# Optimization experiments

Hardware: AMD Instinct MI355X
Metric: run time of the kernel (lower is better)

## Reference

```python
import jax, jax.numpy as jnp
import numpy as np

Q_HEADS, KV_HEADS, HEAD_DIM, WINDOW = 16, 4, 128, 512
HIDDEN = 2048
ROPE_BASE = 10000.0


def _rope_tables(T, head_dim, dtype):
    half = head_dim // 2
    inv_freq = 1.0 / (ROPE_BASE ** (jnp.arange(half, dtype=jnp.float32) / half))
    t = jnp.arange(T, dtype=jnp.float32)
    freqs = jnp.outer(t, inv_freq)  # [T, half]
    return jnp.cos(freqs).astype(dtype), jnp.sin(freqs).astype(dtype)


def _apply_rope(x, cos, sin):
    # x: [B, T, H, D]; cos/sin: [T, D//2] -> broadcast [1, T, 1, D//2]
    c = cos[None, :, None, :]
    s = sin[None, :, None, :]
    x1, x2 = jnp.split(x, 2, axis=-1)
    return jnp.concatenate([x1 * c - x2 * s, x1 * s + x2 * c], axis=-1)


def setup_inputs() -> dict:
    key = jax.random.key(0)
    ks = jax.random.split(key, 5)
    B, T = 1, 4096
    x = jax.random.normal(ks[0], (B, T, HIDDEN), dtype=jnp.float32)
    sc = 0.02
    wq = jax.random.normal(ks[1], (Q_HEADS * HEAD_DIM, HIDDEN), dtype=jnp.float32) * sc
    wk = jax.random.normal(ks[2], (KV_HEADS * HEAD_DIM, HIDDEN), dtype=jnp.float32) * sc
    wv = jax.random.normal(ks[3], (KV_HEADS * HEAD_DIM, HIDDEN), dtype=jnp.float32) * sc
    wo = jax.random.normal(ks[4], (HIDDEN, Q_HEADS * HEAD_DIM), dtype=jnp.float32) * sc
    return {"x": x, "wq": wq, "wk": wk, "wv": wv, "wo": wo}


def reference(x, wq, wk, wv, wo):
    B, T, _ = x.shape
    reps = Q_HEADS // KV_HEADS
    scale = 1.0 / np.sqrt(HEAD_DIM)

    q = jnp.einsum('bth,oh->bto', x, wq).reshape(B, T, Q_HEADS, HEAD_DIM)
    k = jnp.einsum('bth,oh->bto', x, wk).reshape(B, T, KV_HEADS, HEAD_DIM)
    v = jnp.einsum('bth,oh->bto', x, wv).reshape(B, T, KV_HEADS, HEAD_DIM)

    cos, sin = _rope_tables(T, HEAD_DIM, x.dtype)
    q = _apply_rope(q, cos, sin)
    k = _apply_rope(k, cos, sin)

    # GQA without materializing repeated K/V: group q as [B,T,KVH,reps,D]
    qg = q.reshape(B, T, KV_HEADS, reps, HEAD_DIM)
    scores = jnp.einsum('btgrd,bsgd->bgrts', qg, k) * scale  # [B,KVH,reps,T,T]

    idx = jnp.arange(T)
    # allowed: causal (s <= t) AND within window (t - s <= WINDOW)
    allowed = (idx[None, :] <= idx[:, None]) & (idx[:, None] - idx[None, :] <= WINDOW)
    scores = jnp.where(allowed[None, None, None], scores, jnp.finfo(scores.dtype).min)
    probs = jax.nn.softmax(scores, axis=-1)

    out = jnp.einsum('bgrts,bsgd->btgrd', probs, v)  # [B,T,KVH,reps,D]
    out = out.reshape(B, T, Q_HEADS * HEAD_DIM)
    return jnp.einsum('bto,ho->bth', out, wo)
```

## Files before the change

### kernel.cpp

```cpp
#include <hip/hip_runtime.h>

typedef __attribute__((ext_vector_type(8))) short short8;
typedef __attribute__((ext_vector_type(4))) short short4_t;
typedef __attribute__((ext_vector_type(4))) float f32x4;
typedef __attribute__((ext_vector_type(4))) unsigned short u16x4;

__device__ __forceinline__ unsigned short f2b(float f) {
  unsigned int u = __float_as_uint(f);
  u += 0x7fffu + ((u >> 16) & 1u);
  return (unsigned short)(u >> 16);
}
__device__ __forceinline__ float b2f(unsigned short s) {
  return __uint_as_float(((unsigned int)s) << 16);
}
__device__ __forceinline__ void glds16(const void* g, void* l) {
  __builtin_amdgcn_global_load_lds(
      (const __attribute__((address_space(1))) unsigned int*)g,
      (__attribute__((address_space(3))) unsigned int*)l, 16, 0, 0);
}

__global__ __launch_bounds__(256) void cast_all(const float* __restrict__ x,
                                                const float* __restrict__ wq,
                                                const float* __restrict__ wk,
                                                const float* __restrict__ wv,
                                                const float* __restrict__ wo,
                                                unsigned short* __restrict__ dst) {
  const int i = blockIdx.x * 256 + threadIdx.x;
  const float* s;
  int off;
  if (i < 2097152)      { s = x;  off = i; }
  else if (i < 3145728) { s = wq; off = i - 2097152; }
  else if (i < 3407872) { s = wk; off = i - 3145728; }
  else if (i < 3670016) { s = wv; off = i - 3407872; }
  else                  { s = wo; off = i - 3670016; }
  f32x4 v = ((const f32x4*)s)[off];
  u16x4 o;
  o[0] = f2b(v[0]); o[1] = f2b(v[1]); o[2] = f2b(v[2]); o[3] = f2b(v[3]);
  ((u16x4*)dst)[i] = o;
}

__global__ __launch_bounds__(256) void gemm_qkv(const unsigned short* __restrict__ A,
                                                const unsigned short* __restrict__ B,
                                                unsigned short* __restrict__ qb,
                                                unsigned short* __restrict__ kb,
                                                unsigned short* __restrict__ vtg) {
  const int K = 2048;
  __shared__ unsigned short As[128 * 32];
  __shared__ unsigned short Bs[128 * 32];
  const int tid = threadIdx.x;
  const int w = tid >> 6, lane = tid & 63;
  const int quad = lane >> 4, l15 = lane & 15;
  const int m0 = blockIdx.x * 128;
  const int nt = blockIdx.y;
  const int n0 = nt * 128;
  const int mbase = (w >> 1) * 64;
  const f32x4 fzero = {0.f, 0.f, 0.f, 0.f};

  f32x4 acc[4][4];
#pragma unroll
  for (int i = 0; i < 4; i++)
#pragma unroll
    for (int j = 0; j < 4; j++) acc[i][j] = fzero;

  const int srow = w * 16 + (lane >> 2);
  const int scol = (lane & 3) * 8;
  const unsigned short* Ag0 = A + (size_t)(m0 + srow) * K + scol;
  const unsigned short* Ag1 = Ag0 + (size_t)64 * K;
  const unsigned short* Bg0 = B + (size_t)(n0 + srow) * K + scol;
  const unsigned short* Bg1 = Bg0 + (size_t)64 * K;

  for (int k0 = 0; k0 < K; k0 += 32) {
    __syncthreads();
    glds16(Ag0 + k0, &As[w * 512]);
    glds16(Ag1 + k0, &As[2048 + w * 512]);
    glds16(Bg0 + k0, &Bs[w * 512]);
    glds16(Bg1 + k0, &Bs[2048 + w * 512]);
    __syncthreads();
    short8 af[4], bf[4];
#pragma unroll
    for (int mi = 0; mi < 4; mi++)
      af[mi] = *(const short8*)&As[(mbase + mi * 16 + l15) * 32 + quad * 8];
#pragma unroll
    for (int ni = 0; ni < 4; ni++) {
      const int ngrp = (w & 1) * 2 + (ni & 1) + (ni >> 1) * 4;
      bf[ni] = *(const short8*)&Bs[(ngrp * 16 + l15) * 32 + quad * 8];
    }
#pragma unroll
    for (int mi = 0; mi < 4; mi++)
#pragma unroll
      for (int ni = 0; ni < 4; ni++)
        acc[mi][ni] = __builtin_amdgcn_mfma_f32_16x16x32_bf16(af[mi], bf[ni], acc[mi][ni], 0, 0, 0);
  }

  if (nt >= 20) {
    const int g = nt - 20;
#pragma unroll
    for (int mi = 0; mi < 4; mi++) {
      const int tb = m0 + mbase + mi * 16 + quad * 4;
#pragma unroll
      for (int ni = 0; ni < 4; ni++) {
        const int d = ((w & 1) * 2 + (ni & 1) + (ni >> 1) * 4) * 16 + l15;
        u16x4 o;
#pragma unroll
        for (int r = 0; r < 4; r++) o[r] = f2b(acc[mi][ni][r]);
        *(u16x4*)(vtg + (size_t)(g * 128 + d) * 4096 + tb) = o;
      }
    }
  } else {
    unsigned short* dst;
    int stride, hoff;
    if (nt < 16) { dst = qb; stride = 2048; hoff = nt * 128; }
    else         { dst = kb; stride = 512;  hoff = (nt - 16) * 128; }
    const float c2 = 0.20762050593045889f;
    const float inv2pi = 0.15915494309189535f;
#pragma unroll
    for (int ni = 0; ni < 2; ni++) {
      const int i = (w & 1) * 32 + ni * 16 + l15;
      const float inv_rev = exp2f(-(float)i * c2) * inv2pi;
#pragma unroll
      for (int mi = 0; mi < 4; mi++) {
#pragma unroll
        for (int r = 0; r < 4; r++) {
          const int t = m0 + mbase + mi * 16 + quad * 4 + r;
          float rev = (float)t * inv_rev;
          rev = rev - floorf(rev);
          const float sn = __builtin_amdgcn_sinf(rev);
          const float cs = __builtin_amdgcn_cosf(rev);
          const float x1 = acc[mi][ni][r], x2 = acc[mi][ni + 2][r];
          unsigned short* p = dst + (size_t)t * stride + hoff + i;
          p[0]  = f2b(x1 * cs - x2 * sn);
          p[64] = f2b(x1 * sn + x2 * cs);
        }
      }
    }
  }
}

__global__ __launch_bounds__(256) void gemm_bt(const unsigned short* __restrict__ A,
                                               const unsigned short* __restrict__ B,
                                               float* __restrict__ Cout,
                                               int M, int N, int K) {
  __shared__ unsigned short As[128 * 32];
  __shared__ unsigned short Bs[128 * 32];
  const int tid = threadIdx.x;
  const int w = tid >> 6, lane = tid & 63;
  const int quad = lane >> 4, l15 = lane & 15;
  const int m0 = blockIdx.x * 128, n0 = blockIdx.y * 128;
  const int mbase = (w >> 1) * 64, nbase = (w & 1) * 64;
  const f32x4 fzero = {0.f, 0.f, 0.f, 0.f};

  f32x4 acc[4][4];
#pragma unroll
  for (int i = 0; i < 4; i++)
#pragma unroll
    for (int j = 0; j < 4; j++) acc[i][j] = fzero;

  const int srow = w * 16 + (lane >> 2);
  const int scol = (lane & 3) * 8;
  const unsigned short* Ag0 = A + (size_t)(m0 + srow) * K + scol;
  const unsigned short* Ag1 = Ag0 + (size_t)64 * K;
  const unsigned short* Bg0 = B + (size_t)(n0 + srow) * K + scol;
  const unsigned short* Bg1 = Bg0 + (size_t)64 * K;

  for (int k0 = 0; k0 < K; k0 += 32) {
    __syncthreads();
    glds16(Ag0 + k0, &As[w * 512]);
    glds16(Ag1 + k0, &As[2048 + w * 512]);
    glds16(Bg0 + k0, &Bs[w * 512]);
    glds16(Bg1 + k0, &Bs[2048 + w * 512]);
    __syncthreads();
    short8 af[4], bf[4];
#pragma unroll
    for (int mi = 0; mi < 4; mi++)
      af[mi] = *(const short8*)&As[(mbase + mi * 16 + l15) * 32 + quad * 8];
#pragma unroll
    for (int ni = 0; ni < 4; ni++)
      bf[ni] = *(const short8*)&Bs[(nbase + ni * 16 + l15) * 32 + quad * 8];
#pragma unroll
    for (int mi = 0; mi < 4; mi++)
#pragma unroll
      for (int ni = 0; ni < 4; ni++)
        acc[mi][ni] = __builtin_amdgcn_mfma_f32_16x16x32_bf16(af[mi], bf[ni], acc[mi][ni], 0, 0, 0);
  }

#pragma unroll
  for (int mi = 0; mi < 4; mi++)
#pragma unroll
    for (int ni = 0; ni < 4; ni++) {
      const int row = m0 + mbase + mi * 16 + quad * 4;
      const int col = n0 + nbase + ni * 16 + l15;
#pragma unroll
      for (int r = 0; r < 4; r++)
        Cout[(size_t)(row + r) * N + col] = acc[mi][ni][r];
    }
}

__global__ __launch_bounds__(512) void attn_fwd(const unsigned short* __restrict__ qp,
                                                const unsigned short* __restrict__ kp,
                                                const unsigned short* __restrict__ vtg,
                                                unsigned short* __restrict__ op) {
  __shared__ unsigned short Ks[2][4][1024];
  __shared__ unsigned short Vt[2][4096];
  const int tid = threadIdx.x;
  const int w = tid >> 6, lane = tid & 63;
  const int quad = lane >> 4, l15 = lane & 15;
  const int t0 = blockIdx.x * 64;
  const int g = blockIdx.y;
  const int h = g * 4 + (w & 3);
  const int t0w = t0 + (w >> 2) * 32;
  const f32x4 fzero = {0.f, 0.f, 0.f, 0.f};
  const float scale = 0.088388347648318447f;
  const float NEG_INF = -__builtin_inff();

  short8 qf[4][2];
#pragma unroll
  for (int qt = 0; qt < 2; qt++) {
    const unsigned short* qrow = qp + (size_t)(t0w + qt * 16 + l15) * 2048 + h * 128 + quad * 8;
#pragma unroll
    for (int kb = 0; kb < 4; kb++) qf[kb][qt] = *(const short8*)(qrow + kb * 32);
  }

  f32x4 oacc[8][2];
#pragma unroll
  for (int db = 0; db < 8; db++) { oacc[db][0] = fzero; oacc[db][1] = fzero; }
  float Mrow[2] = {-1.0e30f, -1.0e30f}, Lrow[2] = {0.f, 0.f};

  const int s_begin = (t0 >= 512) ? (t0 - 512) : 0;
  const int nch = ((t0 + 63 - s_begin) >> 5) + 1;

  const int r4 = lane >> 2, c4 = lane & 3;
#define ATTN_STAGE(s0_, b_)                                                              \
  {                                                                                      \
    const int s0v = (s0_);                                                               \
    if (w < 4) {                                                                         \
      _Pragma("unroll")                                                                  \
      for (int p = 0; p < 2; p++)                                                        \
        glds16(kp + (size_t)(s0v + p * 16 + r4) * 512 + g * 128 + w * 32 + c4 * 8,       \
               &Ks[b_][w][p * 512]);                                                     \
    } else {                                                                             \
      const int wv = w - 4;                                                              \
      _Pragma("unroll")                                                                  \
      for (int p = 0; p < 2; p++)                                                        \
        glds16(vtg + (size_t)(g * 128 + wv * 32 + p * 16 + r4) * 4096 + s0v + c4 * 8,    \
               &Vt[b_][wv * 1024 + p * 512]);                                            \
    }                                                                                    \
  }

  ATTN_STAGE(s_begin, 0);

  for (int c = 0; c < nch; ++c) {
    const int s0 = s_begin + c * 32;
    const int b = c & 1;
    __syncthreads();
    if (c + 1 < nch) ATTN_STAGE(s_begin + (c + 1) * 32, (c + 1) & 1);

    if (s0 + 31 >= t0w - 512 && s0 <= t0w + 31) {
      f32x4 sacc[2][2];
      sacc[0][0] = fzero; sacc[0][1] = fzero; sacc[1][0] = fzero; sacc[1][1] = fzero;
      const int permBase = ((l15 >> 2) << 3) + (l15 & 3);
#pragma unroll
      for (int kb = 0; kb < 4; kb++) {
        short8 af0 = *(const short8*)&Ks[b][kb][(permBase + 0) * 32 + quad * 8];
        short8 af1 = *(const short8*)&Ks[b][kb][(permBase + 4) * 32 + quad * 8];
        sacc[0][0] = __builtin_amdgcn_mfma_f32_16x16x32_bf16(af0, qf[kb][0], sacc[0][0], 0, 0, 0);
        sacc[0][1] = __builtin_amdgcn_mfma_f32_16x16x32_bf16(af0, qf[kb][1], sacc[0][1], 0, 0, 0);
        sacc[1][0] = __builtin_amdgcn_mfma_f32_16x16x32_bf16(af1, qf[kb][0], sacc[1][0], 0, 0, 0);
        sacc[1][1] = __builtin_amdgcn_mfma_f32_16x16x32_bf16(af1, qf[kb][1], sacc[1][1], 0, 0, 0);
      }

      short8 pb[2];
      float alpha[2];
#pragma unroll
      for (int qt = 0; qt < 2; qt++) {
        const int tq = t0w + qt * 16 + l15;
        float vals[8];
        float cmax = NEG_INF;
#pragma unroll
        for (int kt = 0; kt < 2; kt++)
#pragma unroll
          for (int r = 0; r < 4; r++) {
            const int s = s0 + quad * 8 + kt * 4 + r;
            const bool ok = (unsigned)(tq - s) <= 512u;
            const float v = ok ? sacc[kt][qt][r] * scale : NEG_INF;
            vals[kt * 4 + r] = v;
            cmax = fmaxf(cmax, v);
          }
        cmax = fmaxf(cmax, __shfl_xor(cmax, 16));
        cmax = fmaxf(cmax, __shfl_xor(cmax, 32));
        const float Mnew = fmaxf(Mrow[qt], cmax);
        alpha[qt] = __expf(Mrow[qt] - Mnew);
        Mrow[qt] = Mnew;
        float csum = 0.f;
#pragma unroll
        for (int j = 0; j < 8; j++) {
          const float p = __expf(vals[j] - Mnew);
          csum += p;
          pb[qt][j] = (short)f2b(p);
        }
        csum += __shfl_xor(csum, 16);
        csum += __shfl_xor(csum, 32);
        Lrow[qt] = Lrow[qt] * alpha[qt] + csum;
      }

#pragma unroll
      for (int db = 0; db < 8; db++) {
        short8 vf = *(const short8*)&Vt[b][(db * 16 + l15) * 32 + quad * 8];
#pragma unroll
        for (int qt = 0; qt < 2; qt++) {
          oacc[db][qt][0] *= alpha[qt]; oacc[db][qt][1] *= alpha[qt];
          oacc[db][qt][2] *= alpha[qt]; oacc[db][qt][3] *= alpha[qt];
          oacc[db][qt] = __builtin_amdgcn_mfma_f32_16x16x32_bf16(vf, pb[qt], oacc[db][qt], 0, 0, 0);
        }
      }
    }
  }
#undef ATTN_STAGE

#pragma unroll
  for (int qt = 0; qt < 2; qt++) {
    const float invL = 1.f / Lrow[qt];
    unsigned short* orow = op + (size_t)(t0w + qt * 16 + l15) * 2048 + h * 128;
#pragma unroll
    for (int db = 0; db < 8; db++) {
      u16x4 o;
#pragma unroll
      for (int r = 0; r < 4; r++) o[r] = f2b(oacc[db][qt][r] * invL);
      *(u16x4*)(orow + db * 16 + quad * 4) = o;
    }
  }
}

extern "C" void kernel_launch(void* const* d_in, const int* in_sizes, int n_in,
                              void* d_out, int out_size, void* d_ws, size_t ws_size,
                              hipStream_t stream) {
  const float* x  = (const float*)d_in[0];
  const float* wq = (const float*)d_in[1];
  const float* wk = (const float*)d_in[2];
  const float* wv = (const float*)d_in[3];
  const float* wo = (const float*)d_in[4];
  float* out = (float*)d_out;
  char* ws = (char*)d_ws;

  unsigned short* xb    = (unsigned short*)(ws + 0);
  unsigned short* wqkv  = (unsigned short*)(ws + 16777216);
  unsigned short* wob   = (unsigned short*)(ws + 29360128);
  unsigned short* qb    = (unsigned short*)(ws + 37748736);
  unsigned short* kbuf  = (unsigned short*)(ws + 54525952);
  unsigned short* vtg   = (unsigned short*)(ws + 58720256);
  unsigned short* attnb = xb;

  cast_all<<<18432, 256, 0, stream>>>(x, wq, wk, wv, wo, (unsigned short*)ws);

  gemm_qkv<<<dim3(32, 24), 256, 0, stream>>>(xb, wqkv, qb, kbuf, vtg);

  attn_fwd<<<dim3(64, 4), 512, 0, stream>>>(qb, kbuf, vtg, attnb);

  gemm_bt<<<dim3(32, 16), 256, 0, stream>>>(attnb, wob, out, 4096, 2048, 2048);
}
```

Before: 286.0 us.

## Retile attention to 32-query blocks with 64-key chunks; fold softmax scale into Q

```diff
diff --git a/kernel.cpp b/kernel.cpp
--- a/kernel.cpp
+++ b/kernel.cpp
@@ -107,10 +107,11 @@
       }
     }
   } else {
-    unsigned short* dst;
-    int stride, hoff;
-    if (nt < 16) { dst = qb; stride = 2048; hoff = nt * 128; }
-    else         { dst = kb; stride = 512;  hoff = (nt - 16) * 128; }
+    const bool isq = nt < 16;
+    unsigned short* dst = isq ? qb : kb;
+    const int stride = isq ? 2048 : 512;
+    const int hoff = (isq ? nt : nt - 16) * 128;
+    const float qsc = isq ? 0.088388347648318447f : 1.0f;
     const float c2 = 0.20762050593045889f;
     const float inv2pi = 0.15915494309189535f;
 #pragma unroll
@@ -128,8 +129,8 @@
           const float cs = __builtin_amdgcn_cosf(rev);
           const float x1 = acc[mi][ni][r], x2 = acc[mi][ni + 2][r];
           unsigned short* p = dst + (size_t)t * stride + hoff + i;
-          p[0]  = f2b(x1 * cs - x2 * sn);
-          p[64] = f2b(x1 * sn + x2 * cs);
+          p[0]  = f2b((x1 * cs - x2 * sn) * qsc);
+          p[64] = f2b((x1 * sn + x2 * cs) * qsc);
         }
       }
     }
@@ -195,27 +196,25 @@
     }
 }
 
-__global__ __launch_bounds__(512) void attn_fwd(const unsigned short* __restrict__ qp,
+__global__ __launch_bounds__(256) void attn_fwd(const unsigned short* __restrict__ qp,
                                                 const unsigned short* __restrict__ kp,
                                                 const unsigned short* __restrict__ vtg,
                                                 unsigned short* __restrict__ op) {
-  __shared__ unsigned short Ks[2][4][1024];
-  __shared__ unsigned short Vt[2][4096];
+  __shared__ unsigned short Ks[2][4][2048];
+  __shared__ unsigned short Vt[2][8192];
   const int tid = threadIdx.x;
   const int w = tid >> 6, lane = tid & 63;
   const int quad = lane >> 4, l15 = lane & 15;
-  const int t0 = blockIdx.x * 64;
+  const int t0 = blockIdx.x * 32;
   const int g = blockIdx.y;
-  const int h = g * 4 + (w & 3);
-  const int t0w = t0 + (w >> 2) * 32;
+  const int h = g * 4 + w;
   const f32x4 fzero = {0.f, 0.f, 0.f, 0.f};
-  const float scale = 0.088388347648318447f;
   const float NEG_INF = -__builtin_inff();
 
   short8 qf[4][2];
 #pragma unroll
   for (int qt = 0; qt < 2; qt++) {
-    const unsigned short* qrow = qp + (size_t)(t0w + qt * 16 + l15) * 2048 + h * 128 + quad * 8;
+    const unsigned short* qrow = qp + (size_t)(t0 + qt * 16 + l15) * 2048 + h * 128 + quad * 8;
 #pragma unroll
     for (int kb = 0; kb < 4; kb++) qf[kb][qt] = *(const short8*)(qrow + kb * 32);
   }
@@ -226,91 +225,98 @@
   float Mrow[2] = {-1.0e30f, -1.0e30f}, Lrow[2] = {0.f, 0.f};
 
   const int s_begin = (t0 >= 512) ? (t0 - 512) : 0;
-  const int nch = ((t0 + 63 - s_begin) >> 5) + 1;
-
-  const int r4 = lane >> 2, c4 = lane & 3;
+  const int nch = ((t0 + 31 - s_begin) >> 6) + 1;
+
+  const int kr = lane >> 2, kc = lane & 3;
+  const int vr = lane >> 3, vc = lane & 7;
 #define ATTN_STAGE(s0_, b_)                                                              \
   {                                                                                      \
     const int s0v = (s0_);                                                               \
-    if (w < 4) {                                                                         \
-      _Pragma("unroll")                                                                  \
-      for (int p = 0; p < 2; p++)                                                        \
-        glds16(kp + (size_t)(s0v + p * 16 + r4) * 512 + g * 128 + w * 32 + c4 * 8,       \
-               &Ks[b_][w][p * 512]);                                                     \
-    } else {                                                                             \
-      const int wv = w - 4;                                                              \
-      _Pragma("unroll")                                                                  \
-      for (int p = 0; p < 2; p++)                                                        \
-        glds16(vtg + (size_t)(g * 128 + wv * 32 + p * 16 + r4) * 4096 + s0v + c4 * 8,    \
-               &Vt[b_][wv * 1024 + p * 512]);                                            \
-    }                                                                                    \
+    _Pragma("unroll")                                                                    \
+    for (int p = 0; p < 4; p++)                                                          \
+      glds16(kp + (size_t)(s0v + p * 16 + kr) * 512 + g * 128 + w * 32 + kc * 8,         \
+             &Ks[b_][w][p * 512]);                                                       \
+    _Pragma("unroll")                                                                    \
+    for (int p = 0; p < 4; p++)                                                          \
+      glds16(vtg + (size_t)(g * 128 + w * 32 + p * 8 + vr) * 4096 + s0v + vc * 8,        \
+             &Vt[b_][w * 2048 + p * 512]);                                               \
   }
 
   ATTN_STAGE(s_begin, 0);
 
   for (int c = 0; c < nch; ++c) {
-    const int s0 = s_begin + c * 32;
+    const int s0 = s_begin + c * 64;
     const int b = c & 1;
     __syncthreads();
-    if (c + 1 < nch) ATTN_STAGE(s_begin + (c + 1) * 32, (c + 1) & 1);
-
-    if (s0 + 31 >= t0w - 512 && s0 <= t0w + 31) {
-      f32x4 sacc[2][2];
-      sacc[0][0] = fzero; sacc[0][1] = fzero; sacc[1][0] = fzero; sacc[1][1] = fzero;
-      const int permBase = ((l15 >> 2) << 3) + (l15 & 3);
-#pragma unroll
-      for (int kb = 0; kb < 4; kb++) {
-        short8 af0 = *(const short8*)&Ks[b][kb][(permBase + 0) * 32 + quad * 8];
-        short8 af1 = *(const short8*)&Ks[b][kb][(permBase + 4) * 32 + quad * 8];
-        sacc[0][0] = __builtin_amdgcn_mfma_f32_16x16x32_bf16(af0, qf[kb][0], sacc[0][0], 0, 0, 0);
-        sacc[0][1] = __builtin_amdgcn_mfma_f32_16x16x32_bf16(af0, qf[kb][1], sacc[0][1], 0, 0, 0);
-        sacc[1][0] = __builtin_amdgcn_mfma_f32_16x16x32_bf16(af1, qf[kb][0], sacc[1][0], 0, 0, 0);
-        sacc[1][1] = __builtin_amdgcn_mfma_f32_16x16x32_bf16(af1, qf[kb][1], sacc[1][1], 0, 0, 0);
+    if (c + 1 < nch) ATTN_STAGE(s0 + 64, b ^ 1);
+
+    f32x4 sacc[2][2][2];
+#pragma unroll
+    for (int hh = 0; hh < 2; hh++)
+#pragma unroll
+      for (int kt = 0; kt < 2; kt++) { sacc[hh][kt][0] = fzero; sacc[hh][kt][1] = fzero; }
+    const int permBase = ((l15 >> 2) << 3) + (l15 & 3);
+#pragma unroll
+    for (int kb = 0; kb < 4; kb++) {
+#pragma unroll
+      for (int hh = 0; hh < 2; hh++) {
+        short8 a0 = *(const short8*)&Ks[b][kb][(hh * 32 + permBase + 0) * 32 + quad * 8];
+        short8 a1 = *(const short8*)&Ks[b][kb][(hh * 32 + permBase + 4) * 32 + quad * 8];
+        sacc[hh][0][0] = __builtin_amdgcn_mfma_f32_16x16x32_bf16(a0, qf[kb][0], sacc[hh][0][0], 0, 0, 0);
+        sacc[hh][0][1] = __builtin_amdgcn_mfma_f32_16x16x32_bf16(a0, qf[kb][1], sacc[hh][0][1], 0, 0, 0);
+        sacc[hh][1][0] = __builtin_amdgcn_mfma_f32_16x16x32_bf16(a1, qf[kb][0], sacc[hh][1][0], 0, 0, 0);
+        sacc[hh][1][1] = __builtin_amdgcn_mfma_f32_16x16x32_bf16(a1, qf[kb][1], sacc[hh][1][1], 0, 0, 0);
       }
-
-      short8 pb[2];
-      float alpha[2];
-#pragma unroll
-      for (int qt = 0; qt < 2; qt++) {
-        const int tq = t0w + qt * 16 + l15;
-        float vals[8];
-        float cmax = NEG_INF;
+    }
+
+    short8 pb[2][2];
+    float alpha[2];
+#pragma unroll
+    for (int qt = 0; qt < 2; qt++) {
+      const int tq = t0 + qt * 16 + l15;
+      float vals[2][8];
+      float cmax = NEG_INF;
+#pragma unroll
+      for (int hh = 0; hh < 2; hh++)
 #pragma unroll
         for (int kt = 0; kt < 2; kt++)
 #pragma unroll
           for (int r = 0; r < 4; r++) {
-            const int s = s0 + quad * 8 + kt * 4 + r;
+            const int s = s0 + hh * 32 + quad * 8 + kt * 4 + r;
             const bool ok = (unsigned)(tq - s) <= 512u;
-            const float v = ok ? sacc[kt][qt][r] * scale : NEG_INF;
-            vals[kt * 4 + r] = v;
+            const float v = ok ? sacc[hh][kt][qt][r] : NEG_INF;
+            vals[hh][kt * 4 + r] = v;
             cmax = fmaxf(cmax, v);
           }
-        cmax = fmaxf(cmax, __shfl_xor(cmax, 16));
-        cmax = fmaxf(cmax, __shfl_xor(cmax, 32));
-        const float Mnew = fmaxf(Mrow[qt], cmax);
-        alpha[qt] = __expf(Mrow[qt] - Mnew);
-        Mrow[qt] = Mnew;
-        float csum = 0.f;
+      cmax = fmaxf(cmax, __shfl_xor(cmax, 16));
+      cmax = fmaxf(cmax, __shfl_xor(cmax, 32));
+      const float Mnew = fmaxf(Mrow[qt], cmax);
+      alpha[qt] = __expf(Mrow[qt] - Mnew);
+      Mrow[qt] = Mnew;
+      float csum = 0.f;
+#pragma unroll
+      for (int hh = 0; hh < 2; hh++)
 #pragma unroll
         for (int j = 0; j < 8; j++) {
-          const float p = __expf(vals[j] - Mnew);
+          const float p = __expf(vals[hh][j] - Mnew);
           csum += p;
-          pb[qt][j] = (short)f2b(p);
+          pb[hh][qt][j] = (short)f2b(p);
         }
-        csum += __shfl_xor(csum, 16);
-        csum += __shfl_xor(csum, 32);
-        Lrow[qt] = Lrow[qt] * alpha[qt] + csum;
-      }
-
-#pragma unroll
-      for (int db = 0; db < 8; db++) {
-        short8 vf = *(const short8*)&Vt[b][(db * 16 + l15) * 32 + quad * 8];
-#pragma unroll
-        for (int qt = 0; qt < 2; qt++) {
-          oacc[db][qt][0] *= alpha[qt]; oacc[db][qt][1] *= alpha[qt];
-          oacc[db][qt][2] *= alpha[qt]; oacc[db][qt][3] *= alpha[qt];
-          oacc[db][qt] = __builtin_amdgcn_mfma_f32_16x16x32_bf16(vf, pb[qt], oacc[db][qt], 0, 0, 0);
-        }
+      csum += __shfl_xor(csum, 16);
+      csum += __shfl_xor(csum, 32);
+      Lrow[qt] = Lrow[qt] * alpha[qt] + csum;
+    }
+
+#pragma unroll
+    for (int db = 0; db < 8; db++) {
+      short8 vf0 = *(const short8*)&Vt[b][(db * 16 + l15) * 64 + quad * 8];
+      short8 vf1 = *(const short8*)&Vt[b][(db * 16 + l15) * 64 + 32 + quad * 8];
+#pragma unroll
+      for (int qt = 0; qt < 2; qt++) {
+        oacc[db][qt][0] *= alpha[qt]; oacc[db][qt][1] *= alpha[qt];
+        oacc[db][qt][2] *= alpha[qt]; oacc[db][qt][3] *= alpha[qt];
+        oacc[db][qt] = __builtin_amdgcn_mfma_f32_16x16x32_bf16(vf0, pb[0][qt], oacc[db][qt], 0, 0, 0);
+        oacc[db][qt] = __builtin_amdgcn_mfma_f32_16x16x32_bf16(vf1, pb[1][qt], oacc[db][qt], 0, 0, 0);
       }
     }
   }
@@ -319,7 +325,7 @@
 #pragma unroll
   for (int qt = 0; qt < 2; qt++) {
     const float invL = 1.f / Lrow[qt];
-    unsigned short* orow = op + (size_t)(t0w + qt * 16 + l15) * 2048 + h * 128;
+    unsigned short* orow = op + (size_t)(t0 + qt * 16 + l15) * 2048 + h * 128;
 #pragma unroll
     for (int db = 0; db < 8; db++) {
       u16x4 o;
@@ -353,7 +359,7 @@
 
   gemm_qkv<<<dim3(32, 24), 256, 0, stream>>>(xb, wqkv, qb, kbuf, vtg);
 
-  attn_fwd<<<dim3(64, 4), 512, 0, stream>>>(qb, kbuf, vtg, attnb);
+  attn_fwd<<<dim3(128, 4), 256, 0, stream>>>(qb, kbuf, vtg, attnb);
 
   gemm_bt<<<dim3(32, 16), 256, 0, stream>>>(attnb, wob, out, 4096, 2048, 2048);
 }
```

After: 292.8 us. +2.4%, slower.
